# Optimization experiments

Measured on AMD Instinct MI355X. Metric: run time of the kernel, lower is better.

## Reference

```python
import jax, jax.numpy as jnp
import numpy as np

B, S, D = 4, 2048, 512
H = 8
HD = D // H  # 64


def setup_inputs() -> dict:
    key = jax.random.key(0)
    ks = jax.random.split(key, 11)
    scale = 1.0 / np.sqrt(D)
    inp = {
        "query": jax.random.normal(ks[0], (B, S, D), dtype=jnp.float32),
        "key": jax.random.normal(ks[1], (B, S, D), dtype=jnp.float32),
        "value": jax.random.normal(ks[2], (B, S, D), dtype=jnp.float32),
        "Wq": jax.random.normal(ks[3], (D, D), dtype=jnp.float32) * scale,
        "bq": jnp.zeros((D,), dtype=jnp.float32),
        "Wk": jax.random.normal(ks[4], (D, D), dtype=jnp.float32) * scale,
        "bk": jnp.zeros((D,), dtype=jnp.float32),
        "Wv": jax.random.normal(ks[5], (D, D), dtype=jnp.float32) * scale,
        "bv": jnp.zeros((D,), dtype=jnp.float32),
        "Wo": jax.random.normal(ks[6], (D, D), dtype=jnp.float32) * scale,
        "bo": jnp.zeros((D,), dtype=jnp.float32),
    }
    return inp


def reference(query, key, value, Wq, bq, Wk, bk, Wv, bv, Wo, bo):
    # Linear projections (torch Linear: x @ W.T + b)
    q = (query @ Wq.T + bq).reshape(B, -1, H, HD).transpose(0, 2, 1, 3)  # [B,H,Sq,HD]
    k = (key   @ Wk.T + bk).reshape(B, -1, H, HD).transpose(0, 2, 1, 3)  # [B,H,Sk,HD]
    v = (value @ Wv.T + bv).reshape(B, -1, H, HD).transpose(0, 2, 1, 3)  # [B,H,Sk,HD]

    # Chunked loop in original is mathematically identical to full attention
    scores = jnp.einsum('bhqd,bhkd->bhqk', q, k) / np.sqrt(HD)  # [B,H,Sq,Sk]
    attn = jax.nn.softmax(scores, axis=-1)
    out = jnp.einsum('bhqk,bhkd->bhqd', attn, v)  # [B,H,Sq,HD]
    out = out.transpose(0, 2, 1, 3).reshape(B, -1, D)  # [B,Sq,D]
    return out @ Wo.T + bo
```

## Files before the change

kernel.cpp:

```cpp
#include <hip/hip_runtime.h>
#include <hip/hip_bf16.h>

typedef __attribute__((ext_vector_type(8))) short bf16x8;
typedef __attribute__((ext_vector_type(4))) float f32x4;
typedef __attribute__((ext_vector_type(16))) float f32x16;
typedef __attribute__((ext_vector_type(4))) unsigned int u32x4;

#define MFMA16(a, b, c) __builtin_amdgcn_mfma_f32_16x16x32_bf16((a), (b), (c), 0, 0, 0)
#define MFMA32(a, b, c) __builtin_amdgcn_mfma_f32_32x32x16_bf16((a), (b), (c), 0, 0, 0)

static constexpr int BATCH = 4, S = 2048, DMODEL = 512, H = 8, HD = 64;
static constexpr int M = BATCH * S;

#define WAIT_VM(N) asm volatile("s_waitcnt vmcnt(" #N ")" ::: "memory")
#define SCHEDB() __builtin_amdgcn_sched_barrier(0)

__device__ __forceinline__ float rexp2(float x) {
  float r;
  asm("v_exp_f32 %0, %1" : "=v"(r) : "v"(x));
  return r;
}

__device__ __forceinline__ short f2b(float f) {
  unsigned int u = __builtin_bit_cast(unsigned int, f);
  unsigned int r = (u + 0x7fffu + ((u >> 16) & 1u)) >> 16;
  return (short)r;
}

__device__ __forceinline__ bf16x8 cvt8(const float4& a, const float4& b) {
  bf16x8 r;
  r[0] = f2b(a.x); r[1] = f2b(a.y); r[2] = f2b(a.z); r[3] = f2b(a.w);
  r[4] = f2b(b.x); r[5] = f2b(b.y); r[6] = f2b(b.z); r[7] = f2b(b.w);
  return r;
}

__device__ __forceinline__ void glds16(const void* g, void* l) {
  __builtin_amdgcn_global_load_lds(
      (const __attribute__((address_space(1))) unsigned int*)g,
      (__attribute__((address_space(3))) unsigned int*)l, 16, 0, 0);
}

__global__ __launch_bounds__(256) void convert_all(
    const float* __restrict__ q, const float* __restrict__ k, const float* __restrict__ v,
    const float* __restrict__ Wq, const float* __restrict__ Wk,
    const float* __restrict__ Wv, const float* __restrict__ Wo,
    short* __restrict__ Abq, short* __restrict__ Abk, short* __restrict__ Abv,
    short* __restrict__ Wb) {
  const int bid = blockIdx.x;
  const float* src;
  short* dst;
  int i;
  if (bid < 6144) {
    const int which = bid >> 11;
    const int sub = bid & 2047;
    src = (which == 0) ? q : (which == 1) ? k : v;
    dst = (which == 0) ? Abq : (which == 1) ? Abk : Abv;
    i = (sub * 256 + threadIdx.x) * 8;
  } else {
    const int wb = bid - 6144;
    const int which = wb >> 7;
    const int sub = wb & 127;
    src = (which == 0) ? Wq : (which == 1) ? Wk : (which == 2) ? Wv : Wo;
    dst = Wb + which * (DMODEL * DMODEL);
    i = (sub * 256 + threadIdx.x) * 8;
  }
  float4 a = *(const float4*)&src[i];
  float4 b = *(const float4*)&src[i + 4];
  *(bf16x8*)&dst[i] = cvt8(a, b);
}

__global__ __launch_bounds__(256) void proj_gemm(
    const short* __restrict__ Abq, const short* __restrict__ Abk, const short* __restrict__ Abv,
    const short* __restrict__ Wb,
    const float* __restrict__ bq, const float* __restrict__ bk, const float* __restrict__ bv,
    short* __restrict__ Qp, short* __restrict__ Kp, short* __restrict__ Vp) {
  const int which = blockIdx.y;
  const short* A    = (which == 0) ? Abq : (which == 1) ? Abk : Abv;
  const short* W    = Wb + which * (DMODEL * DMODEL);
  const float* bias = (which == 0) ? bq : (which == 1) ? bk : bv;
  short* dst        = (which == 0) ? Qp : (which == 1) ? Kp : Vp;

  const int tm = blockIdx.x & 63;
  const int tn = blockIdx.x >> 6;
  const int m0 = tm * 128, n0 = tn * 128;
  const int t = threadIdx.x;
  const int lane = t & 63, w = t >> 6;
  const int g = lane >> 4, c = lane & 15;
  const int wr = w >> 1, wc = w & 1;

  __shared__ __align__(16) short SM[3][2 * 128 * 32];

  f32x4 acc[4][4];
  const f32x4 fz = {0.f, 0.f, 0.f, 0.f};
#pragma unroll
  for (int i = 0; i < 4; ++i)
#pragma unroll
    for (int j = 0; j < 4; ++j) acc[i][j] = fz;

  const short* Asrc0 = A + (m0 + w * 16 + (lane >> 2)) * DMODEL + (lane & 3) * 8;
  const short* Asrc1 = Asrc0 + 64 * DMODEL;
  const short* Bsrc0 = W + (n0 + w * 16 + (lane >> 2)) * DMODEL + (lane & 3) * 8;
  const short* Bsrc1 = Bsrc0 + 64 * DMODEL;

#pragma unroll
  for (int tt = 0; tt < 2; ++tt) {
    glds16(Asrc0 + tt * 32, &SM[tt][w * 512]);
    glds16(Asrc1 + tt * 32, &SM[tt][2048 + w * 512]);
    glds16(Bsrc0 + tt * 32, &SM[tt][4096 + w * 512]);
    glds16(Bsrc1 + tt * 32, &SM[tt][4096 + 2048 + w * 512]);
  }

  int ob0 = 0, ob1 = 1, ob2 = 2;
  for (int kt = 0; kt < 16; ++kt) {
    if (kt == 15) { WAIT_VM(0); } else { WAIT_VM(4); }
    __builtin_amdgcn_s_barrier();
    SCHEDB();
    if (kt < 14) {
      const int k0 = (kt + 2) * 32;
      glds16(Asrc0 + k0, &SM[ob2][w * 512]);
      glds16(Asrc1 + k0, &SM[ob2][2048 + w * 512]);
      glds16(Bsrc0 + k0, &SM[ob2][4096 + w * 512]);
      glds16(Bsrc1 + k0, &SM[ob2][4096 + 2048 + w * 512]);
    }
    SCHEDB();

    bf16x8 af[4], bfr[4];
#pragma unroll
    for (int i = 0; i < 4; ++i)
      af[i] = *(const bf16x8*)&SM[ob0][(wr * 64 + i * 16 + c) * 32 + g * 8];
#pragma unroll
    for (int j = 0; j < 4; ++j)
      bfr[j] = *(const bf16x8*)&SM[ob0][4096 + (wc * 64 + j * 16 + c) * 32 + g * 8];
    if (which == 2) {
#pragma unroll
      for (int i = 0; i < 4; ++i)
#pragma unroll
        for (int j = 0; j < 4; ++j)
          acc[i][j] = MFMA16(bfr[j], af[i], acc[i][j]);
    } else {
#pragma unroll
      for (int i = 0; i < 4; ++i)
#pragma unroll
        for (int j = 0; j < 4; ++j)
          acc[i][j] = MFMA16(af[i], bfr[j], acc[i][j]);
    }

    const int tmp = ob0; ob0 = ob1; ob1 = ob2; ob2 = tmp;
  }

  if (which == 2) {
#pragma unroll
    for (int j = 0; j < 4; ++j) {
#pragma unroll
      for (int r = 0; r < 4; ++r) {
        const int n = n0 + wc * 64 + j * 16 + g * 4 + r;
        const int h = n >> 6, hd = n & 63;
        const float bn = bias[n];
#pragma unroll
        for (int i = 0; i < 4; ++i) {
          const int m = m0 + wr * 64 + i * 16 + c;
          const int bb = m >> 11, s = m & (S - 1);
          dst[((bb * H + h) * HD + hd) * S + s] = f2b(acc[i][j][r] + bn);
        }
      }
    }
  } else {
#pragma unroll
    for (int i = 0; i < 4; ++i) {
#pragma unroll
      for (int j = 0; j < 4; ++j) {
        const int n = n0 + wc * 64 + j * 16 + c;
        const int h = n >> 6, hd = n & 63;
        const float bn = bias[n];
#pragma unroll
        for (int r = 0; r < 4; ++r) {
          const int m = m0 + wr * 64 + i * 16 + g * 4 + r;
          const int bb = m >> 11, s = m & (S - 1);
          dst[((bb * H + h) * S + s) * HD + hd] = f2b(acc[i][j][r] + bn);
        }
      }
    }
  }
}

__global__ __launch_bounds__(256) void out_gemm(
    const short* __restrict__ Am, const short* __restrict__ W,
    const float* __restrict__ bias, float* __restrict__ Out) {
  const int tm = blockIdx.x & 63;
  const int tn = blockIdx.x >> 6;
  const int m0 = tm * 128, n0 = tn * 128;
  const int t = threadIdx.x;
  const int lane = t & 63, w = t >> 6;
  const int g = lane >> 4, c = lane & 15;
  const int wr = w >> 1, wc = w & 1;

  __shared__ __align__(16) short SM[3][2 * 128 * 32];

  f32x4 acc[4][4];
  const f32x4 fz = {0.f, 0.f, 0.f, 0.f};
#pragma unroll
  for (int i = 0; i < 4; ++i)
#pragma unroll
    for (int j = 0; j < 4; ++j) acc[i][j] = fz;

  const short* Asrc0 = Am + (m0 + w * 16 + (lane >> 2)) * DMODEL + (lane & 3) * 8;
  const short* Asrc1 = Asrc0 + 64 * DMODEL;
  const short* Bsrc0 = W + (n0 + w * 16 + (lane >> 2)) * DMODEL + (lane & 3) * 8;
  const short* Bsrc1 = Bsrc0 + 64 * DMODEL;

#pragma unroll
  for (int tt = 0; tt < 2; ++tt) {
    glds16(Asrc0 + tt * 32, &SM[tt][w * 512]);
    glds16(Asrc1 + tt * 32, &SM[tt][2048 + w * 512]);
    glds16(Bsrc0 + tt * 32, &SM[tt][4096 + w * 512]);
    glds16(Bsrc1 + tt * 32, &SM[tt][4096 + 2048 + w * 512]);
  }

  int ob0 = 0, ob1 = 1, ob2 = 2;
  for (int kt = 0; kt < 16; ++kt) {
    if (kt == 15) { WAIT_VM(0); } else { WAIT_VM(4); }
    __builtin_amdgcn_s_barrier();
    SCHEDB();
    if (kt < 14) {
      const int k0 = (kt + 2) * 32;
      glds16(Asrc0 + k0, &SM[ob2][w * 512]);
      glds16(Asrc1 + k0, &SM[ob2][2048 + w * 512]);
      glds16(Bsrc0 + k0, &SM[ob2][4096 + w * 512]);
      glds16(Bsrc1 + k0, &SM[ob2][4096 + 2048 + w * 512]);
    }
    SCHEDB();

    bf16x8 af[4], bfr[4];
#pragma unroll
    for (int i = 0; i < 4; ++i)
      af[i] = *(const bf16x8*)&SM[ob0][(wr * 64 + i * 16 + c) * 32 + g * 8];
#pragma unroll
    for (int j = 0; j < 4; ++j)
      bfr[j] = *(const bf16x8*)&SM[ob0][4096 + (wc * 64 + j * 16 + c) * 32 + g * 8];
#pragma unroll
    for (int i = 0; i < 4; ++i)
#pragma unroll
      for (int j = 0; j < 4; ++j)
        acc[i][j] = MFMA16(af[i], bfr[j], acc[i][j]);

    const int tmp = ob0; ob0 = ob1; ob1 = ob2; ob2 = tmp;
  }

#pragma unroll
  for (int i = 0; i < 4; ++i) {
#pragma unroll
    for (int j = 0; j < 4; ++j) {
      const int n = n0 + wc * 64 + j * 16 + c;
      const float bn = bias[n];
#pragma unroll
      for (int r = 0; r < 4; ++r) {
        const int m = m0 + wr * 64 + i * 16 + g * 4 + r;
        Out[m * DMODEL + n] = acc[i][j][r] + bn;
      }
    }
  }
}

__global__ __launch_bounds__(256, 2) void attn_kernel(
    const short* __restrict__ Qp, const short* __restrict__ Kp,
    const short* __restrict__ VTp, short* __restrict__ att) {
  const int bid = blockIdx.x;
  const int swzb = (bid & 7) * 64 + (bid >> 3);
  const int qt = swzb & 15;
  const int bh = swzb >> 4;
  const int b = bh >> 3, h = bh & 7;
  const short* Q  = Qp  + bh * (S * HD);
  const char*  Kg = (const char*)(Kp  + bh * (S * HD));
  const char*  Vg = (const char*)(VTp + bh * (HD * S));

  const int t = threadIdx.x;
  const int lane = t & 63, w = t >> 6;
  const int l31 = lane & 31, hi = lane >> 5;
  const int q0 = qt * 128 + w * 32;

  __shared__ __align__(16) char smem[2 * 32768];

  const int rowi = lane >> 3;
  const char* ksrc = Kg + (w * 32 + rowi) * 128 + (((lane & 7) * 16) ^ (rowi << 4));
  const int vrow = lane >> 4;
  const char* vsrc[4];
#pragma unroll
  for (int j = 0; j < 4; ++j)
    vsrc[j] = Vg + (w * 16 + j * 4 + vrow) * 4096 +
              (((lane & 15) * 16) ^ (((j * 4 + vrow) & 7) << 4));

  bf16x8 qf[4];
#pragma unroll
  for (int ks = 0; ks < 4; ++ks)
    qf[ks] = *(const bf16x8*)&Q[(q0 + l31) * HD + ks * 16 + hi * 8];

  bf16x8 ones;
#pragma unroll
  for (int i = 0; i < 8; ++i) ones[i] = (short)0x3F80;

  f32x16 o0, o1, osum, fz16;
#pragma unroll
  for (int i = 0; i < 16; ++i) { o0[i] = 0.f; o1[i] = 0.f; osum[i] = 0.f; fz16[i] = 0.f; }

  const float SCL = 0.18033688011112042f;
  const int fswz = (l31 & 7) << 4;

  {
    char* nb = smem;
#pragma unroll
    for (int j = 0; j < 4; ++j) glds16(ksrc + j * 1024, nb + w * 4096 + j * 1024);
#pragma unroll
    for (int j = 0; j < 4; ++j) glds16(vsrc[j], nb + 16384 + w * 4096 + j * 1024);
  }

  for (int kt = 0; kt < 16; ++kt) {
    WAIT_VM(0);
    __builtin_amdgcn_s_barrier();
    SCHEDB();
    if (kt < 15) {
      char* nb = smem + ((kt + 1) & 1) * 32768;
      const size_t ko = (size_t)(kt + 1) * 16384;
      const size_t vo = (size_t)(kt + 1) * 256;
#pragma unroll
      for (int j = 0; j < 4; ++j) glds16(ksrc + ko + j * 1024, nb + w * 4096 + j * 1024);
#pragma unroll
      for (int j = 0; j < 4; ++j) glds16(vsrc[j] + vo, nb + 16384 + w * 4096 + j * 1024);
    }
    SCHEDB();

    const int cb = (kt & 1) * 32768;
#pragma unroll
    for (int hb = 0; hb < 2; ++hb) {
      const int kvb = cb + hb * 64 * 128;
      f32x16 sa0, sa1;
      __builtin_amdgcn_s_setprio(1);
      {
        const int col0 = (hi * 16) ^ fswz;
        const bf16x8 k00 = *(const bf16x8*)&smem[kvb + l31 * 128 + col0];
        const bf16x8 k10 = *(const bf16x8*)&smem[kvb + (32 + l31) * 128 + col0];
        sa0 = MFMA32(k00, qf[0], fz16);
        sa1 = MFMA32(k10, qf[0], fz16);
      }
#pragma unroll
      for (int ks = 1; ks < 4; ++ks) {
        const int col = (ks * 32 + hi * 16) ^ fswz;
        const bf16x8 k0 = *(const bf16x8*)&smem[kvb + l31 * 128 + col];
        const bf16x8 k1 = *(const bf16x8*)&smem[kvb + (32 + l31) * 128 + col];
        sa0 = MFMA32(k0, qf[ks], sa0);
        sa1 = MFMA32(k1, qf[ks], sa1);
      }
      __builtin_amdgcn_s_setprio(0);

#pragma unroll
      for (int i = 0; i < 16; ++i) {
        sa0[i] = rexp2(sa0[i] * SCL);
        sa1[i] = rexp2(sa1[i] * SCL);
      }

      unsigned int wrd0[8], wrd1[8];
#pragma unroll
      for (int i = 0; i < 8; ++i) {
        asm("v_cvt_pk_bf16_f32 %0, %1, %2" : "=v"(wrd0[i]) : "v"(sa0[2 * i]), "v"(sa0[2 * i + 1]));
        asm("v_cvt_pk_bf16_f32 %0, %1, %2" : "=v"(wrd1[i]) : "v"(sa1[2 * i]), "v"(sa1[2 * i + 1]));
      }

      __builtin_amdgcn_s_setprio(1);
#pragma unroll
      for (int ks = 0; ks < 4; ++ks) {
        const int i0 = (ks & 1) * 4;
        unsigned int a0 = (ks < 2) ? wrd0[i0 + 0] : wrd1[i0 + 0];
        unsigned int b0 = (ks < 2) ? wrd0[i0 + 2] : wrd1[i0 + 2];
        unsigned int a1 = (ks < 2) ? wrd0[i0 + 1] : wrd1[i0 + 1];
        unsigned int b1 = (ks < 2) ? wrd0[i0 + 3] : wrd1[i0 + 3];
        asm("v_permlane32_swap_b32 %0, %1" : "+v"(a0), "+v"(b0));
        asm("v_permlane32_swap_b32 %0, %1" : "+v"(a1), "+v"(b1));
        u32x4 fw;
        fw[0] = a0; fw[1] = a1; fw[2] = b0; fw[3] = b1;
        const bf16x8 pfrag = __builtin_bit_cast(bf16x8, fw);
        const int colv = (hb * 128 + ks * 32 + hi * 16) ^ fswz;
        const bf16x8 va0 = *(const bf16x8*)&smem[cb + 16384 + l31 * 256 + colv];
        const bf16x8 va1 = *(const bf16x8*)&smem[cb + 16384 + (32 + l31) * 256 + colv];
        o0 = MFMA32(va0, pfrag, o0);
        o1 = MFMA32(va1, pfrag, o1);
        osum = MFMA32(ones, pfrag, osum);
      }
      __builtin_amdgcn_s_setprio(0);
    }
  }

  const float inv = 1.0f / osum[0];
  short* arow = att + (b * S + q0 + l31) * DMODEL + h * HD;
#pragma unroll
  for (int dt = 0; dt < 2; ++dt) {
#pragma unroll
    for (int rr = 0; rr < 4; ++rr) {
      float v0 = (dt ? o1[4 * rr + 0] : o0[4 * rr + 0]) * inv;
      float v1 = (dt ? o1[4 * rr + 1] : o0[4 * rr + 1]) * inv;
      float v2 = (dt ? o1[4 * rr + 2] : o0[4 * rr + 2]) * inv;
      float v3 = (dt ? o1[4 * rr + 3] : o0[4 * rr + 3]) * inv;
      unsigned int w0, w1;
      asm("v_cvt_pk_bf16_f32 %0, %1, %2" : "=v"(w0) : "v"(v0), "v"(v1));
      asm("v_cvt_pk_bf16_f32 %0, %1, %2" : "=v"(w1) : "v"(v2), "v"(v3));
      uint2 pk2;
      pk2.x = w0; pk2.y = w1;
      *(uint2*)&arow[dt * 32 + rr * 8 + hi * 4] = pk2;
    }
  }
}

extern "C" void kernel_launch(void* const* d_in, const int* in_sizes, int n_in,
                              void* d_out, int out_size, void* d_ws, size_t ws_size,
                              hipStream_t stream) {
  const float* query = (const float*)d_in[0];
  const float* key_  = (const float*)d_in[1];
  const float* value = (const float*)d_in[2];
  const float* Wq = (const float*)d_in[3];
  const float* bq = (const float*)d_in[4];
  const float* Wk = (const float*)d_in[5];
  const float* bk = (const float*)d_in[6];
  const float* Wv = (const float*)d_in[7];
  const float* bv = (const float*)d_in[8];
  const float* Wo = (const float*)d_in[9];
  const float* bo = (const float*)d_in[10];
  float* out = (float*)d_out;

  char* ws = (char*)d_ws;
  const size_t WB_BYTES  = (size_t)4 * DMODEL * DMODEL * 2;
  const size_t MAT_BYTES = (size_t)M * DMODEL * 2;
  short* Wb  = (short*)ws;
  short* Qp  = (short*)(ws + WB_BYTES);
  short* Kp  = (short*)(ws + WB_BYTES + MAT_BYTES);
  short* Vp  = (short*)(ws + WB_BYTES + 2 * MAT_BYTES);
  short* att = (short*)(ws + WB_BYTES + 3 * MAT_BYTES);
  short* Abq = (short*)(ws + WB_BYTES + 4 * MAT_BYTES);
  short* Abk = (short*)(ws + WB_BYTES + 5 * MAT_BYTES);
  short* Abv = att;

  convert_all<<<dim3(6656), 256, 0, stream>>>(query, key_, value, Wq, Wk, Wv, Wo,
                                              Abq, Abk, Abv, Wb);
  proj_gemm<<<dim3(256, 3), 256, 0, stream>>>(Abq, Abk, Abv, Wb, bq, bk, bv, Qp, Kp, Vp);
  attn_kernel<<<dim3(512), 256, 0, stream>>>(Qp, Kp, Vp, att);
  out_gemm<<<dim3(256), 256, 0, stream>>>(att, Wb + 3 * DMODEL * DMODEL, bo, out);
}
```

Before: 95.06 us.

## Replace ones-MFMA row sum with VALU reduction and process full KV tile at once

Removes the extra MFMA against a vector of ones that accumulated the softmax denominator, and computes the row sum instead by adding the fp32 exponentials on the VALU with a cross-half shuffle. The two half-tile iterations are merged so four score tiles are computed and exponentiated together before the PV MFMAs. This cuts MFMA work by a third in the PV stage. In exchange it raises register pressure and VALU work, and the denominator now sums fp32 values instead of the bf16-rounded probabilities used in the numerator.

Result: no change. 93.95 us (-1.2%).

```diff
diff --git a/kernel.cpp b/kernel.cpp
--- a/kernel.cpp
+++ b/kernel.cpp
@@ -294,13 +294,10 @@
   for (int ks = 0; ks < 4; ++ks)
     qf[ks] = *(const bf16x8*)&Q[(q0 + l31) * HD + ks * 16 + hi * 8];
 
-  bf16x8 ones;
-#pragma unroll
-  for (int i = 0; i < 8; ++i) ones[i] = (short)0x3F80;
-
-  f32x16 o0, o1, osum, fz16;
-#pragma unroll
-  for (int i = 0; i < 16; ++i) { o0[i] = 0.f; o1[i] = 0.f; osum[i] = 0.f; fz16[i] = 0.f; }
+  f32x16 o0, o1, fz16;
+#pragma unroll
+  for (int i = 0; i < 16; ++i) { o0[i] = 0.f; o1[i] = 0.f; fz16[i] = 0.f; }
+  float lst = 0.f;
 
   const float SCL = 0.18033688011112042f;
   const int fswz = (l31 & 7) << 4;
@@ -329,66 +326,77 @@
     SCHEDB();
 
     const int cb = (kt & 1) * 32768;
-#pragma unroll
-    for (int hb = 0; hb < 2; ++hb) {
-      const int kvb = cb + hb * 64 * 128;
-      f32x16 sa0, sa1;
-      __builtin_amdgcn_s_setprio(1);
-      {
-        const int col0 = (hi * 16) ^ fswz;
-        const bf16x8 k00 = *(const bf16x8*)&smem[kvb + l31 * 128 + col0];
-        const bf16x8 k10 = *(const bf16x8*)&smem[kvb + (32 + l31) * 128 + col0];
-        sa0 = MFMA32(k00, qf[0], fz16);
-        sa1 = MFMA32(k10, qf[0], fz16);
-      }
-#pragma unroll
-      for (int ks = 1; ks < 4; ++ks) {
-        const int col = (ks * 32 + hi * 16) ^ fswz;
-        const bf16x8 k0 = *(const bf16x8*)&smem[kvb + l31 * 128 + col];
-        const bf16x8 k1 = *(const bf16x8*)&smem[kvb + (32 + l31) * 128 + col];
-        sa0 = MFMA32(k0, qf[ks], sa0);
-        sa1 = MFMA32(k1, qf[ks], sa1);
-      }
-      __builtin_amdgcn_s_setprio(0);
-
-#pragma unroll
-      for (int i = 0; i < 16; ++i) {
-        sa0[i] = rexp2(sa0[i] * SCL);
-        sa1[i] = rexp2(sa1[i] * SCL);
-      }
-
-      unsigned int wrd0[8], wrd1[8];
-#pragma unroll
-      for (int i = 0; i < 8; ++i) {
-        asm("v_cvt_pk_bf16_f32 %0, %1, %2" : "=v"(wrd0[i]) : "v"(sa0[2 * i]), "v"(sa0[2 * i + 1]));
-        asm("v_cvt_pk_bf16_f32 %0, %1, %2" : "=v"(wrd1[i]) : "v"(sa1[2 * i]), "v"(sa1[2 * i + 1]));
-      }
-
-      __builtin_amdgcn_s_setprio(1);
-#pragma unroll
-      for (int ks = 0; ks < 4; ++ks) {
-        const int i0 = (ks & 1) * 4;
-        unsigned int a0 = (ks < 2) ? wrd0[i0 + 0] : wrd1[i0 + 0];
-        unsigned int b0 = (ks < 2) ? wrd0[i0 + 2] : wrd1[i0 + 2];
-        unsigned int a1 = (ks < 2) ? wrd0[i0 + 1] : wrd1[i0 + 1];
-        unsigned int b1 = (ks < 2) ? wrd0[i0 + 3] : wrd1[i0 + 3];
-        asm("v_permlane32_swap_b32 %0, %1" : "+v"(a0), "+v"(b0));
-        asm("v_permlane32_swap_b32 %0, %1" : "+v"(a1), "+v"(b1));
-        u32x4 fw;
-        fw[0] = a0; fw[1] = a1; fw[2] = b0; fw[3] = b1;
-        const bf16x8 pfrag = __builtin_bit_cast(bf16x8, fw);
-        const int colv = (hb * 128 + ks * 32 + hi * 16) ^ fswz;
-        const bf16x8 va0 = *(const bf16x8*)&smem[cb + 16384 + l31 * 256 + colv];
-        const bf16x8 va1 = *(const bf16x8*)&smem[cb + 16384 + (32 + l31) * 256 + colv];
-        o0 = MFMA32(va0, pfrag, o0);
-        o1 = MFMA32(va1, pfrag, o1);
-        osum = MFMA32(ones, pfrag, osum);
-      }
-      __builtin_amdgcn_s_setprio(0);
-    }
-  }
-
-  const float inv = 1.0f / osum[0];
+
+    f32x16 sA, sB, sC, sD;
+    __builtin_amdgcn_s_setprio(1);
+    {
+      const int col0 = (hi * 16) ^ fswz;
+      sA = MFMA32(*(const bf16x8*)&smem[cb + l31 * 128 + col0],          qf[0], fz16);
+      sB = MFMA32(*(const bf16x8*)&smem[cb + (32 + l31) * 128 + col0],   qf[0], fz16);
+      sC = MFMA32(*(const bf16x8*)&smem[cb + 8192 + l31 * 128 + col0],   qf[0], fz16);
+      sD = MFMA32(*(const bf16x8*)&smem[cb + 8192 + (32 + l31) * 128 + col0], qf[0], fz16);
+    }
+#pragma unroll
+    for (int ks = 1; ks < 4; ++ks) {
+      const int col = (ks * 32 + hi * 16) ^ fswz;
+      sA = MFMA32(*(const bf16x8*)&smem[cb + l31 * 128 + col],          qf[ks], sA);
+      sB = MFMA32(*(const bf16x8*)&smem[cb + (32 + l31) * 128 + col],   qf[ks], sB);
+      sC = MFMA32(*(const bf16x8*)&smem[cb + 8192 + l31 * 128 + col],   qf[ks], sC);
+      sD = MFMA32(*(const bf16x8*)&smem[cb + 8192 + (32 + l31) * 128 + col], qf[ks], sD);
+    }
+    __builtin_amdgcn_s_setprio(0);
+
+#pragma unroll
+    for (int i = 0; i < 16; ++i) {
+      sA[i] = rexp2(sA[i] * SCL);
+      sB[i] = rexp2(sB[i] * SCL);
+      sC[i] = rexp2(sC[i] * SCL);
+      sD[i] = rexp2(sD[i] * SCL);
+    }
+
+    float ts[16];
+#pragma unroll
+    for (int i = 0; i < 16; ++i) ts[i] = (sA[i] + sB[i]) + (sC[i] + sD[i]);
+#pragma unroll
+    for (int i = 0; i < 8; ++i) ts[i] = ts[i] + ts[i + 8];
+#pragma unroll
+    for (int i = 0; i < 4; ++i) ts[i] = ts[i] + ts[i + 4];
+    ts[0] = (ts[0] + ts[2]) + (ts[1] + ts[3]);
+    lst += ts[0] + __shfl_xor(ts[0], 32, 64);
+
+    unsigned int wrdA[8], wrdB[8], wrdC[8], wrdD[8];
+#pragma unroll
+    for (int i = 0; i < 8; ++i) {
+      asm("v_cvt_pk_bf16_f32 %0, %1, %2" : "=v"(wrdA[i]) : "v"(sA[2 * i]), "v"(sA[2 * i + 1]));
+      asm("v_cvt_pk_bf16_f32 %0, %1, %2" : "=v"(wrdB[i]) : "v"(sB[2 * i]), "v"(sB[2 * i + 1]));
+      asm("v_cvt_pk_bf16_f32 %0, %1, %2" : "=v"(wrdC[i]) : "v"(sC[2 * i]), "v"(sC[2 * i + 1]));
+      asm("v_cvt_pk_bf16_f32 %0, %1, %2" : "=v"(wrdD[i]) : "v"(sD[2 * i]), "v"(sD[2 * i + 1]));
+    }
+
+    __builtin_amdgcn_s_setprio(1);
+#pragma unroll
+    for (int ss = 0; ss < 8; ++ss) {
+      const int ks = ss & 3;
+      const int i0 = (ks & 1) * 4;
+      const unsigned int* lo = (ss < 4) ? ((ks < 2) ? wrdA : wrdB)
+                                        : ((ks < 2) ? wrdC : wrdD);
+      unsigned int a0 = lo[i0 + 0], b0 = lo[i0 + 2];
+      unsigned int a1 = lo[i0 + 1], b1 = lo[i0 + 3];
+      asm("v_permlane32_swap_b32 %0, %1" : "+v"(a0), "+v"(b0));
+      asm("v_permlane32_swap_b32 %0, %1" : "+v"(a1), "+v"(b1));
+      u32x4 fw;
+      fw[0] = a0; fw[1] = a1; fw[2] = b0; fw[3] = b1;
+      const bf16x8 pfrag = __builtin_bit_cast(bf16x8, fw);
+      const int colv = (ss * 32 + hi * 16) ^ fswz;
+      const bf16x8 va0 = *(const bf16x8*)&smem[cb + 16384 + l31 * 256 + colv];
+      const bf16x8 va1 = *(const bf16x8*)&smem[cb + 16384 + (32 + l31) * 256 + colv];
+      o0 = MFMA32(va0, pfrag, o0);
+      o1 = MFMA32(va1, pfrag, o1);
+    }
+    __builtin_amdgcn_s_setprio(0);
+  }
+
+  const float inv = 1.0f / lst;
   short* arow = att + (b * S + q0 + l31) * DMODEL + h * HD;
 #pragma unroll
   for (int dt = 0; dt < 2; ++dt) {
```
